# Kernel optimization log

Hardware: AMD Instinct MI355X
Metric: run time of the kernel (lower is better)

## Reference

```python
import jax, jax.numpy as jnp
import numpy as np

B, L, D, ORDER, POS, HID, LMAX = 4, 4096, 1024, 2, 65, 64, 4096
K2 = (POS - 1) // 2

def _layernorm(x, w, b, eps=1e-5):
    m = jnp.mean(x, -1, keepdims=True)
    v = jnp.mean((x - m) ** 2, -1, keepdims=True)
    return (x - m) * jax.lax.rsqrt(v + eps) * w + b

def _fftconv(x, h, d):
    # torch: rfft(h, 2L, norm='forward') * rfft(x, 2L) -> irfft(.., norm='forward')
    # net scaling equals standard (unnormalized fwd / 1-over-n inverse) circular conv,
    # which is exactly jnp.fft default conventions.
    n = 2 * x.shape[-1]
    y = jnp.fft.irfft(jnp.fft.rfft(x, n=n) * jnp.fft.rfft(h, n=n), n=n)[..., : x.shape[-1]]
    return y + x * d

def setup_inputs() -> dict:
    key = jax.random.key(0)
    ks = jax.random.split(key, 12)
    s = 0.05
    # PositionalEncoding buffers/params (deterministic init, as in torch __init__)
    t = np.linspace(0, 1, LMAX, dtype=np.float64)[:, None]
    t_pos = np.arange(LMAX, dtype=np.float64)[:, None]
    k = np.arange(K2, dtype=np.float64)[None, :]
    z = np.exp(1j * 2 * np.pi * k * t_pos / LMAX)
    pos_z = np.concatenate([t, z.real, z.imag], axis=-1).astype(np.float32)  # (LMAX, POS)
    pos_t = t.reshape(1, 1, LMAX).astype(np.float32)
    # ExponentialDecayWindow alphas (deterministic init)
    max_decay = np.log(0.01) / 0.3
    min_decay = np.log(0.01) / 1.5
    alphas = np.linspace(min_decay, max_decay, D).reshape(1, D, 1).astype(np.float32)
    H3 = (ORDER + 1) * D
    return dict(
        u=jax.random.normal(ks[0], (B, L, D), jnp.float32),
        norm1_w=jnp.ones((D,), jnp.float32), norm1_b=jnp.zeros((D,), jnp.float32),
        proj_w=jax.random.normal(ks[1], (H3, D), jnp.float32) * s,
        proj_b=jnp.zeros((H3,), jnp.float32),
        conv_w=jax.random.normal(ks[2], (H3, 1, 3), jnp.float32) * 0.3,
        conv_b=jnp.zeros((H3,), jnp.float32),
        pos_t=jnp.asarray(pos_t), pos_z=jnp.asarray(pos_z),
        fnn_w0=jax.random.normal(ks[3], (HID, POS), jnp.float32) * s,
        fnn_b0=jnp.zeros((HID,), jnp.float32),
        freq0=8.0 * jnp.ones((1, HID), jnp.float32),
        fnn_w1=jax.random.normal(ks[4], (HID, HID), jnp.float32) * s,
        fnn_b1=jnp.zeros((HID,), jnp.float32),
        freq1=8.0 * jnp.ones((1, HID), jnp.float32),
        fnn_w2=jax.random.normal(ks[5], (HID, HID), jnp.float32) * s,
        fnn_b2=jnp.zeros((HID,), jnp.float32),
        freq2=8.0 * jnp.ones((1, HID), jnp.float32),
        fnn_wout=jax.random.normal(ks[6], (ORDER * D, HID), jnp.float32) * s,
        alphas=jnp.asarray(alphas),
        hy_bias=jax.random.normal(ks[7], (ORDER, 1, D, 1), jnp.float32),
        norm2_w=jnp.ones((D,), jnp.float32), norm2_b=jnp.zeros((D,), jnp.float32),
        fc_w=jax.random.normal(ks[8], (D, D), jnp.float32) * s,
        fc_b=jnp.zeros((D,), jnp.float32),
    )

def reference(u, norm1_w, norm1_b, proj_w, proj_b, conv_w, conv_b, pos_t, pos_z,
              fnn_w0, fnn_b0, freq0, fnn_w1, fnn_b1, freq1, fnn_w2, fnn_b2, freq2,
              fnn_wout, alphas, hy_bias, norm2_w, norm2_b, fc_w, fc_b):
    Lq = u.shape[1]
    # Projection: LN -> Linear -> depthwise short conv (causal-ish, pad=2, slice :L)
    x = _layernorm(u, norm1_w, norm1_b)
    x = jnp.einsum('bld,hd->blh', x, proj_w) + proj_b          # (B,L,3D)
    x = x.transpose(0, 2, 1)                                   # (B,3D,L)
    x = jax.lax.conv_general_dilated(
        x, conv_w, window_strides=(1,), padding=[(2, 2)],
        feature_group_count=x.shape[1],
        dimension_numbers=('NCH', 'OIH', 'NCH'))[..., :Lq] + conv_b[None, :, None]
    # HyenaFilter: sin-MLP over positional features, then exp-decay window
    zf = pos_z[:Lq]                                            # (L,POS)
    h = jnp.sin(freq0 * (zf @ fnn_w0.T + fnn_b0))
    h = jnp.sin(freq1 * (h @ fnn_w1.T + fnn_b1))
    h = jnp.sin(freq2 * (h @ fnn_w2.T + fnn_b2))
    h = (h @ fnn_wout.T).T.reshape(ORDER, D, Lq)               # (order,D,L)
    decay = jnp.exp(alphas * pos_t[..., :Lq])                  # (1,D,L)
    h = h * decay
    # order-wise gated FFT long convolution (faithful to torch chunk/broadcast semantics)
    v = x[:, -1:, :]                                           # (B,1,L)
    for i in range(ORDER):
        v = x[:, i:i + 1, :] * _fftconv(v, h[i][None], hy_bias[i])  # (B,D,L)
    y = u + v.transpose(0, 2, 1)
    out = _layernorm(y, norm2_w, norm2_b) @ fc_w.T + fc_b      # activation = identity
    return out + y
```

## Files before the change

### kernel.cpp

```cpp
#include <hip/hip_runtime.h>
#include <hip/hip_bf16.h>

#define LL 4096
#define DD 1024
#define NB 4
#define N4 4096
#define KBINS 4097
#define NSLOT4 4366
#define PI_F 3.14159265358979323846f
#define INV4 (1.0f / 4096.0f)

typedef __attribute__((ext_vector_type(4))) float f32x4;
typedef __attribute__((ext_vector_type(8))) short s16x8;

__device__ __forceinline__ unsigned short f2bf(float f) {
  unsigned int x = __float_as_uint(f);
  x += 0x7fffu + ((x >> 16) & 1u);
  return (unsigned short)(x >> 16);
}

__device__ __forceinline__ int SLT(int n) { return n + (n >> 4) + (n >> 8); }
__device__ __forceinline__ int brev12(int n) { return (int)(__brev((unsigned)n) >> 20); }

__device__ __forceinline__ float2 cmul(float2 a, float2 b) {
  return make_float2(a.x * b.x - a.y * b.y, a.x * b.y + a.y * b.x);
}
__device__ __forceinline__ float2 cadd(float2 a, float2 b) { return make_float2(a.x + b.x, a.y + b.y); }
__device__ __forceinline__ float2 csub(float2 a, float2 b) { return make_float2(a.x - b.x, a.y - b.y); }
__device__ __forceinline__ float2 conjf(float2 a) { return make_float2(a.x, -a.y); }
__device__ __forceinline__ float2 mulni(float2 v) { return make_float2(v.y, -v.x); }
__device__ __forceinline__ float2 mulpi(float2 v) { return make_float2(-v.y, v.x); }

__global__ void k_twiddle(float2* tw) {
  int k = blockIdx.x * 256 + threadIdx.x;
  if (k < 4096) {
    float ang = -2.0f * PI_F * (float)k / 8192.0f;
    float s, c;
    sincosf(ang, &s, &c);
    tw[k] = make_float2(c, s);
  }
}

template<bool INV>
__device__ __forceinline__ void bfly8(float2& A0, float2& A1, float2& A2, float2& A3,
                                      float2& A4, float2& A5, float2& A6, float2& A7,
                                      float2 w1, float2 w2, float2 w3) {
  const float C8 = 0.70710678118654752f;
  float2 t;
  t = cmul(w1, A1); float2 b0 = cadd(A0, t), b1 = csub(A0, t);
  t = cmul(w1, A3); float2 b2 = cadd(A2, t), b3 = csub(A2, t);
  t = cmul(w1, A5); float2 b4 = cadd(A4, t), b5 = csub(A4, t);
  t = cmul(w1, A7); float2 b6 = cadd(A6, t), b7 = csub(A6, t);
  t = cmul(w2, b2);                     float2 c0 = cadd(b0, t), c2 = csub(b0, t);
  t = cmul(w2, b3); t = INV ? mulpi(t) : mulni(t);
  float2 c1 = cadd(b1, t), c3 = csub(b1, t);
  t = cmul(w2, b6);                     float2 c4 = cadd(b4, t), c6 = csub(b4, t);
  t = cmul(w2, b7); t = INV ? mulpi(t) : mulni(t);
  float2 c5 = cadd(b5, t), c7 = csub(b5, t);
  t = cmul(w3, c4); A0 = cadd(c0, t); A4 = csub(c0, t);
  float2 e1 = cmul(w3, c5);
  t = INV ? make_float2(C8 * (e1.x - e1.y), C8 * (e1.y + e1.x))
          : make_float2(C8 * (e1.x + e1.y), C8 * (e1.y - e1.x));
  A1 = cadd(c1, t); A5 = csub(c1, t);
  float2 e2 = cmul(w3, c6); t = INV ? mulpi(e2) : mulni(e2);
  A2 = cadd(c2, t); A6 = csub(c2, t);
  float2 e3 = cmul(w3, c7);
  t = INV ? make_float2(-C8 * (e3.x + e3.y), C8 * (e3.x - e3.y))
          : make_float2(C8 * (e3.y - e3.x), -C8 * (e3.x + e3.y));
  A3 = cadd(c3, t); A7 = csub(c3, t);
}

template<bool INV>
__device__ __forceinline__ void fft4k_01(float2* Z, const float2* __restrict__ tw) {
  const int tid = threadIdx.x;
#pragma unroll
  for (int p = 0; p < 3; ++p) {
    const int hs = 3 * p;
    const int h = 1 << hs;
    const int j0 = tid & (h - 1);
    const int i = ((tid >> hs) << (hs + 3)) + j0;
    int s0 = SLT(i),         s1 = SLT(i + h),     s2 = SLT(i + 2 * h), s3 = SLT(i + 3 * h);
    int s4 = SLT(i + 4 * h), s5 = SLT(i + 5 * h), s6 = SLT(i + 6 * h), s7 = SLT(i + 7 * h);
    float2 a0 = Z[s0], a1 = Z[s1], a2 = Z[s2], a3 = Z[s3];
    float2 a4 = Z[s4], a5 = Z[s5], a6 = Z[s6], a7 = Z[s7];
    float2 w1 = tw[j0 << (12 - hs)];
    float2 w2 = tw[j0 << (11 - hs)];
    float2 w3 = tw[j0 << (10 - hs)];
    if (INV) { w1.y = -w1.y; w2.y = -w2.y; w3.y = -w3.y; }
    bfly8<INV>(a0, a1, a2, a3, a4, a5, a6, a7, w1, w2, w3);
    Z[s0] = a0; Z[s1] = a1; Z[s2] = a2; Z[s3] = a3;
    Z[s4] = a4; Z[s5] = a5; Z[s6] = a6; Z[s7] = a7;
    __builtin_amdgcn_wave_barrier();
  }
}

template<bool INV>
__device__ __forceinline__ void fft4k_p3(const float2* Z, const float2* __restrict__ tw,
                                         float2 d[8]) {
  const int t = threadIdx.x;
#pragma unroll
  for (int k = 0; k < 8; ++k) d[k] = Z[SLT(t + 512 * k)];
  float2 w1 = tw[t << 3], w2 = tw[t << 2], w3 = tw[t << 1];
  if (INV) { w1.y = -w1.y; w2.y = -w2.y; w3.y = -w3.y; }
  bfly8<INV>(d[0], d[1], d[2], d[3], d[4], d[5], d[6], d[7], w1, w2, w3);
}

__global__ __launch_bounds__(256) void k_ln_proj(
    const float* __restrict__ u, const float* __restrict__ n1w, const float* __restrict__ n1b,
    const float* __restrict__ pw, const float* __restrict__ pb,
    float* __restrict__ xp0, float* __restrict__ xp1, float* __restrict__ xpL) {
  const int wid = threadIdx.x >> 6, lane = threadIdx.x & 63;
  const int r = blockIdx.x * 4 + wid;
  const float* ur = u + (size_t)r * DD;
  float4 uv[4];
  float s = 0.f, sq = 0.f;
#pragma unroll
  for (int c = 0; c < 4; ++c) {
    uv[c] = ((const float4*)ur)[lane + 64 * c];
    s += uv[c].x + uv[c].y + uv[c].z + uv[c].w;
    sq += uv[c].x * uv[c].x + uv[c].y * uv[c].y + uv[c].z * uv[c].z + uv[c].w * uv[c].w;
  }
  for (int m = 1; m < 64; m <<= 1) { s += __shfl_xor(s, m); sq += __shfl_xor(sq, m); }
  const float mean = s * (1.0f / DD);
  const float var = sq * (1.0f / DD) - mean * mean;
  const float rs = rsqrtf(var + 1e-5f);
  float d0 = 0.f, d1 = 0.f, dL = 0.f;
  const float* pwL = pw + (size_t)3071 * DD;
#pragma unroll
  for (int c = 0; c < 4; ++c) {
    int i4 = lane + 64 * c;
    float4 wv = ((const float4*)n1w)[i4];
    float4 bv = ((const float4*)n1b)[i4];
    float4 p0 = ((const float4*)pw)[i4];
    float4 p1v = ((const float4*)(pw + DD))[i4];
    float4 pLv = ((const float4*)pwL)[i4];
    float xn;
    xn = (uv[c].x - mean) * rs * wv.x + bv.x; d0 += xn * p0.x; d1 += xn * p1v.x; dL += xn * pLv.x;
    xn = (uv[c].y - mean) * rs * wv.y + bv.y; d0 += xn * p0.y; d1 += xn * p1v.y; dL += xn * pLv.y;
    xn = (uv[c].z - mean) * rs * wv.z + bv.z; d0 += xn * p0.z; d1 += xn * p1v.z; dL += xn * pLv.z;
    xn = (uv[c].w - mean) * rs * wv.w + bv.w; d0 += xn * p0.w; d1 += xn * p1v.w; dL += xn * pLv.w;
  }
  for (int m = 1; m < 64; m <<= 1) {
    d0 += __shfl_xor(d0, m); d1 += __shfl_xor(d1, m); dL += __shfl_xor(dL, m);
  }
  if (lane == 0) {
    xp0[r] = d0 + pb[0];
    xp1[r] = d1 + pb[1];
    xpL[r] = dL + pb[3071];
  }
}

__global__ __launch_bounds__(256) void k_tapconv(
    const float* __restrict__ xp0, const float* __restrict__ xp1, const float* __restrict__ xpL,
    const float* __restrict__ cw, const float* __restrict__ cb,
    float* __restrict__ x0c, float* __restrict__ x1c, float* __restrict__ xLc) {
  int idx = blockIdx.x * 256 + threadIdx.x;
  if (idx >= NB * LL) return;
  int l = idx & (LL - 1);
  int base = idx - l;
  {
    const float* a = xp0 + base;
    float v = cw[2] * a[l];
    if (l >= 1) v += cw[1] * a[l - 1];
    if (l >= 2) v += cw[0] * a[l - 2];
    x0c[idx] = v + cb[0];
  }
  {
    const float* a = xp1 + base;
    float v = cw[5] * a[l];
    if (l >= 1) v += cw[4] * a[l - 1];
    if (l >= 2) v += cw[3] * a[l - 2];
    x1c[idx] = v + cb[1];
  }
  {
    const float* a = xpL + base;
    float v = cw[3071 * 3 + 2] * a[l];
    if (l >= 1) v += cw[3071 * 3 + 1] * a[l - 1];
    if (l >= 2) v += cw[3071 * 3 + 0] * a[l - 2];
    xLc[idx] = v + cb[3071];
  }
}

__global__ __launch_bounds__(256) void k_ffn_hidden(
    const float* __restrict__ pos_z,
    const float* __restrict__ w0, const float* __restrict__ b0, const float* __restrict__ f0,
    const float* __restrict__ w1, const float* __restrict__ b1, const float* __restrict__ f1,
    const float* __restrict__ w2, const float* __restrict__ b2, const float* __restrict__ f2,
    float* __restrict__ hid2T) {
  __shared__ float zin[4][66];
  __shared__ float hbuf[4][64];
  const int g = threadIdx.x >> 6, lane = threadIdx.x & 63;
  const int l0 = blockIdx.x * 16;
  for (int it = 0; it < 4; ++it) {
    const int l = l0 + g * 4 + it;
    zin[g][lane] = pos_z[(size_t)l * 65 + lane];
    if (lane == 0) zin[g][64] = pos_z[(size_t)l * 65 + 64];
    __syncthreads();
    float acc = b0[lane];
#pragma unroll
    for (int k = 0; k < 65; ++k) acc += zin[g][k] * w0[lane * 65 + k];
    float hv = sinf(f0[lane] * acc);
    __syncthreads();
    hbuf[g][lane] = hv;
    __syncthreads();
    acc = b1[lane];
#pragma unroll
    for (int k = 0; k < 64; ++k) acc += hbuf[g][k] * w1[lane * 64 + k];
    hv = sinf(f1[lane] * acc);
    __syncthreads();
    hbuf[g][lane] = hv;
    __syncthreads();
    acc = b2[lane];
#pragma unroll
    for (int k = 0; k < 64; ++k) acc += hbuf[g][k] * w2[lane * 64 + k];
    hv = sinf(f2[lane] * acc);
    hid2T[(size_t)lane * LL + l] = hv;
    __syncthreads();
  }
}

__global__ __launch_bounds__(512, 4) void k_fft_filters(
    const float* __restrict__ hid2T, const float* __restrict__ wout,
    const float* __restrict__ alphas, const float* __restrict__ pos_t,
    float2* __restrict__ Hs, const float2* __restrict__ tw) {
  __shared__ float2 Z[NSLOT4];
  __shared__ float wd[64];
  const int i = blockIdx.x >> 10, d = blockIdx.x & 1023;
  const int tid = threadIdx.x;
  if (tid < 64) wd[tid] = wout[(size_t)(i * DD + d) * 64 + tid];
  __syncthreads();
  const float ad = alphas[d];
  const float2* h2 = (const float2*)hid2T;
  const float2* pt2 = (const float2*)pos_t;
#pragma unroll
  for (int gi = 0; gi < 4; ++gi) {
    int j = tid + gi * 512;
    float2 acc = make_float2(0.f, 0.f);
#pragma unroll 16
    for (int k = 0; k < 64; ++k) {
      float2 hv = h2[(size_t)k * 2048 + j];
      acc.x = fmaf(hv.x, wd[k], acc.x);
      acc.y = fmaf(hv.y, wd[k], acc.y);
    }
    float2 tt = pt2[j];
    float2 val = make_float2(acc.x * expf(ad * tt.x), acc.y * expf(ad * tt.y));
    int r = brev12(j);
    Z[SLT(r)] = val;
    Z[SLT(r + 1)] = make_float2(0.f, 0.f);
  }
  __syncthreads();
  fft4k_01<false>(Z, tw);
  __syncthreads();
  float2 dd[8];
  fft4k_p3<false>(Z, tw, dd);
#pragma unroll
  for (int k = 0; k < 8; ++k) Z[SLT(tid + 512 * k)] = dd[k];
  __syncthreads();
  float2* O1 = Hs + ((size_t)i * DD + d) * KBINS;
#pragma unroll
  for (int gi = 0; gi < 4; ++gi) {
    int k = tid + gi * 512;
    float2 zk = Z[SLT(k)];
    float2 zm = Z[SLT((N4 - k) & (N4 - 1))];
    float2 B = conjf(zm);
    float2 E = make_float2(0.5f * (zk.x + B.x), 0.5f * (zk.y + B.y));
    float2 F = make_float2(0.5f * (zk.x - B.x), 0.5f * (zk.y - B.y));
    float2 G = cmul(tw[k], F);
    float2 WO = mulni(G);
    O1[k] = cadd(E, WO);
    O1[N4 - k] = conjf(csub(E, WO));
  }
  if (tid == 0) {
    float2 zc = Z[SLT(2048)];
    float2 F = make_float2(0.f, zc.y);
    float2 G = cmul(tw[2048], F);
    O1[2048] = cadd(make_float2(zc.x, 0.f), mulni(G));
  }
}

__global__ __launch_bounds__(512, 4) void k_fft_v0(const float* __restrict__ xLc,
                                                   float2* __restrict__ V0s,
                                                   const float2* __restrict__ tw) {
  __shared__ float2 Z[NSLOT4];
  const int b = blockIdx.x;
  const int tid = threadIdx.x;
  const float2* src = (const float2*)(xLc + (size_t)b * LL);
#pragma unroll
  for (int gi = 0; gi < 4; ++gi) {
    int j = tid + gi * 512;
    float2 v = src[j];
    int r = brev12(j);
    Z[SLT(r)] = v;
    Z[SLT(r + 1)] = make_float2(0.f, 0.f);
  }
  __syncthreads();
  fft4k_01<false>(Z, tw);
  __syncthreads();
  float2 dd[8];
  fft4k_p3<false>(Z, tw, dd);
#pragma unroll
  for (int k = 0; k < 8; ++k) Z[SLT(tid + 512 * k)] = dd[k];
  __syncthreads();
  float2* Va = V0s + (size_t)b * KBINS;
#pragma unroll
  for (int gi = 0; gi < 4; ++gi) {
    int k = tid + gi * 512;
    float2 zk = Z[SLT(k)];
    float2 zm = Z[SLT((N4 - k) & (N4 - 1))];
    float2 B = conjf(zm);
    float2 E = make_float2(0.5f * (zk.x + B.x), 0.5f * (zk.y + B.y));
    float2 F = make_float2(0.5f * (zk.x - B.x), 0.5f * (zk.y - B.y));
    float2 G = cmul(tw[k], F);
    float2 WO = mulni(G);
    Va[k] = cadd(E, WO);
    Va[N4 - k] = conjf(csub(E, WO));
  }
  if (tid == 0) {
    float2 zc = Z[SLT(2048)];
    float2 F = make_float2(0.f, zc.y);
    float2 G = cmul(tw[2048], F);
    Va[2048] = cadd(make_float2(zc.x, 0.f), mulni(G));
  }
}

__global__ __launch_bounds__(512, 4) void k_conv12(
    const float2* __restrict__ Hs, const float2* __restrict__ V0s,
    const float* __restrict__ x0c, const float* __restrict__ x1c, const float* __restrict__ xLc,
    const float* __restrict__ hyb, float* __restrict__ v2, const float2* __restrict__ tw) {
  __shared__ float2 Z[NSLOT4];
  const int b = blockIdx.x >> 10, d = blockIdx.x & 1023;
  const int tid = threadIdx.x;
  const float2* H0 = Hs + (size_t)d * KBINS;
  const float2* H1 = Hs + (size_t)(DD + d) * KBINS;
  const float2* V = V0s + (size_t)b * KBINS;
#pragma unroll
  for (int gi = 0; gi < 4; ++gi) {
    int k = tid + gi * 512;
    int m = N4 - k;
    float2 Yk = cmul(V[k], H0[k]);
    float2 Ym = cmul(V[m], H0[m]);
    float2 B = conjf(Ym);
    float2 E = make_float2(0.5f * (Yk.x + B.x), 0.5f * (Yk.y + B.y));
    float2 F = make_float2(0.5f * (Yk.x - B.x), 0.5f * (Yk.y - B.y));
    float2 O = cmul(conjf(tw[k]), F);
    float2 iO = mulpi(O);
    Z[SLT(brev12(k))] = cadd(E, iO);
    if (k > 0) Z[SLT(brev12(m))] = conjf(csub(E, iO));
  }
  if (tid == 0) {
    float2 A = cmul(V[2048], H0[2048]);
    float2 F = make_float2(0.f, A.y);
    float2 O = cmul(conjf(tw[2048]), F);
    Z[SLT(brev12(2048))] = cadd(make_float2(A.x, 0.f), mulpi(O));
  }
  __syncthreads();
  fft4k_01<true>(Z, tw);
  __syncthreads();
  float2 dA[8];
  fft4k_p3<true>(Z, tw, dA);
  const float bd0 = hyb[d], bd1 = hyb[DD + d];
  const float2* g0 = (const float2*)(x0c + (size_t)b * LL);
  const float2* g1 = (const float2*)(x1c + (size_t)b * LL);
  const float2* v0 = (const float2*)(xLc + (size_t)b * LL);
  float2 vsave[4];
#pragma unroll
  for (int k = 0; k < 4; ++k) {
    int j = tid + 512 * k;
    float2 gg = g0[j], vv = v0[j];
    vsave[k] = make_float2(gg.x * fmaf(dA[k].x, INV4, bd0 * vv.x),
                           gg.y * fmaf(dA[k].y, INV4, bd0 * vv.y));
  }
  __syncthreads();
#pragma unroll
  for (int k = 0; k < 4; ++k) {
    int j = tid + 512 * k;
    int r = brev12(j);
    Z[SLT(r)] = vsave[k];
    Z[SLT(r + 1)] = make_float2(0.f, 0.f);
  }
  __syncthreads();
  fft4k_01<false>(Z, tw);
  __syncthreads();
  float2 dB[8];
  fft4k_p3<false>(Z, tw, dB);
#pragma unroll
  for (int k = 0; k < 8; ++k) Z[SLT(tid + 512 * k)] = dB[k];
  __syncthreads();
  float2 zpk[4], zpm[4], z2048;
#pragma unroll
  for (int gi = 0; gi < 4; ++gi) {
    int k = tid + gi * 512;
    int m = N4 - k;
    float2 zk = Z[SLT(k)];
    float2 zm = Z[SLT(m & (N4 - 1))];
    float2 B = conjf(zm);
    float2 E = make_float2(0.5f * (zk.x + B.x), 0.5f * (zk.y + B.y));
    float2 F = make_float2(0.5f * (zk.x - B.x), 0.5f * (zk.y - B.y));
    float2 wk = tw[k];
    float2 G = cmul(wk, F);
    float2 WO = mulni(G);
    float2 Xk = cadd(E, WO);
    float2 Xm = conjf(csub(E, WO));
    float2 Yk = cmul(Xk, H1[k]);
    float2 Ym = cmul(Xm, H1[m]);
    float2 B2 = conjf(Ym);
    float2 E2 = make_float2(0.5f * (Yk.x + B2.x), 0.5f * (Yk.y + B2.y));
    float2 F2 = make_float2(0.5f * (Yk.x - B2.x), 0.5f * (Yk.y - B2.y));
    float2 O2 = cmul(conjf(wk), F2);
    float2 iO2 = mulpi(O2);
    zpk[gi] = cadd(E2, iO2);
    zpm[gi] = conjf(csub(E2, iO2));
  }
  if (tid == 0) {
    float2 zc = Z[SLT(2048)];
    float2 F = make_float2(0.f, zc.y);
    float2 G = cmul(tw[2048], F);
    float2 Xk = cadd(make_float2(zc.x, 0.f), mulni(G));
    float2 Y = cmul(Xk, H1[2048]);
    float2 F2 = make_float2(0.f, Y.y);
    float2 O2 = cmul(conjf(tw[2048]), F2);
    z2048 = cadd(make_float2(Y.x, 0.f), mulpi(O2));
  }
  __syncthreads();
#pragma unroll
  for (int gi = 0; gi < 4; ++gi) {
    int k = tid + gi * 512;
    Z[SLT(brev12(k))] = zpk[gi];
    if (k > 0) Z[SLT(brev12(N4 - k))] = zpm[gi];
  }
  if (tid == 0) Z[SLT(brev12(2048))] = z2048;
  __syncthreads();
  fft4k_01<true>(Z, tw);
  __syncthreads();
  float2 dC[8];
  fft4k_p3<true>(Z, tw, dC);
  float2* out2 = (float2*)(v2 + ((size_t)b * DD + d) * LL);
#pragma unroll
  for (int k = 0; k < 4; ++k) {
    int j = tid + 512 * k;
    float2 gg = g1[j];
    out2[j] = make_float2(gg.x * fmaf(dC[k].x, INV4, bd1 * vsave[k].x),
                          gg.y * fmaf(dC[k].y, INV4, bd1 * vsave[k].y));
  }
}

__global__ __launch_bounds__(256) void k_transpose_add(const float* __restrict__ v2,
                                                       const float* __restrict__ u,
                                                       float* __restrict__ y) {
  __shared__ float T[64][65];
  const int bid = blockIdx.x;
  const int lt = bid & 63, dt = (bid >> 6) & 15, b = bid >> 10;
  const int t = threadIdx.x;
  const int tdr = t >> 2, lc0 = (t & 3) * 16;
  const float* vp = v2 + ((size_t)(b * DD + dt * 64 + tdr)) * LL + lt * 64 + lc0;
#pragma unroll
  for (int q = 0; q < 4; ++q) {
    float4 vv = ((const float4*)vp)[q];
    T[tdr][lc0 + 4 * q + 0] = vv.x;
    T[tdr][lc0 + 4 * q + 1] = vv.y;
    T[tdr][lc0 + 4 * q + 2] = vv.z;
    T[tdr][lc0 + 4 * q + 3] = vv.w;
  }
  __syncthreads();
  const int dc = t & 63, lg = t >> 6;
#pragma unroll
  for (int lr0 = 0; lr0 < 64; lr0 += 4) {
    int lr = lr0 + lg;
    size_t idx = ((size_t)b * LL + lt * 64 + lr) * DD + dt * 64 + dc;
    y[idx] = u[idx] + T[dc][lr];
  }
}

__global__ __launch_bounds__(256) void k_ln2(const float* __restrict__ y,
                                             const float* __restrict__ w,
                                             const float* __restrict__ bb,
                                             unsigned short* __restrict__ yln) {
  const int wid = threadIdx.x >> 6, lane = threadIdx.x & 63;
  const size_t r = (size_t)blockIdx.x * 4 + wid;
  const float* yr = y + r * DD;
  float4 v[4];
  float s = 0.f, sq = 0.f;
#pragma unroll
  for (int c = 0; c < 4; ++c) {
    v[c] = ((const float4*)yr)[lane + 64 * c];
    s += v[c].x + v[c].y + v[c].z + v[c].w;
    sq += v[c].x * v[c].x + v[c].y * v[c].y + v[c].z * v[c].z + v[c].w * v[c].w;
  }
  for (int m = 1; m < 64; m <<= 1) { s += __shfl_xor(s, m); sq += __shfl_xor(sq, m); }
  const float mean = s * (1.0f / DD);
  const float var = sq * (1.0f / DD) - mean * mean;
  const float rs = rsqrtf(var + 1e-5f);
#pragma unroll
  for (int c = 0; c < 4; ++c) {
    int i4 = lane + 64 * c;
    float4 wv = ((const float4*)w)[i4];
    float4 bv = ((const float4*)bb)[i4];
    ushort4 o;
    o.x = f2bf((v[c].x - mean) * rs * wv.x + bv.x);
    o.y = f2bf((v[c].y - mean) * rs * wv.y + bv.y);
    o.z = f2bf((v[c].z - mean) * rs * wv.z + bv.z);
    o.w = f2bf((v[c].w - mean) * rs * wv.w + bv.w);
    ((ushort4*)(yln + r * DD))[i4] = o;
  }
}

__global__ void k_cast(const float* __restrict__ src, unsigned short* __restrict__ dst, int n4) {
  int i = blockIdx.x * 256 + threadIdx.x;
  if (i < n4) {
    float4 v = ((const float4*)src)[i];
    ushort4 o;
    o.x = f2bf(v.x); o.y = f2bf(v.y); o.z = f2bf(v.z); o.w = f2bf(v.w);
    ((ushort4*)dst)[i] = o;
  }
}

#define GBM 128
#define GBN 128
#define GBK 64
#define LDKP 72

__global__ __launch_bounds__(256) void k_gemm(const short* __restrict__ A,
                                              const short* __restrict__ Bw,
                                              const float* __restrict__ fcb,
                                              const float* __restrict__ yy,
                                              float* __restrict__ out) {
  __shared__ short As[GBM * LDKP];
  __shared__ short Bs[GBN * LDKP];
  const int t = threadIdx.x;
  const int bm = blockIdx.x & 127;
  const int bn = blockIdx.x >> 7;
  const int wave = t >> 6, lane = t & 63;
  const int wr = wave >> 1, wc = wave & 1;
  const int rrow = lane & 15, kb = (lane >> 4) * 8;

  f32x4 acc[4][4];
#pragma unroll
  for (int i = 0; i < 4; ++i)
#pragma unroll
    for (int j = 0; j < 4; ++j) acc[i][j] = (f32x4){0.f, 0.f, 0.f, 0.f};

  for (int k0 = 0; k0 < 1024; k0 += GBK) {
#pragma unroll
    for (int c = 0; c < 4; ++c) {
      int chunk = c * 256 + t;
      int row = chunk >> 3, off = (chunk & 7) * 8;
      s16x8 av = *(const s16x8*)(A + ((size_t)(bm * GBM + row)) * 1024 + k0 + off);
      *(s16x8*)&As[row * LDKP + off] = av;
      s16x8 bv = *(const s16x8*)(Bw + ((size_t)(bn * GBN + row)) * 1024 + k0 + off);
      *(s16x8*)&Bs[row * LDKP + off] = bv;
    }
    __syncthreads();
    s16x8 af[2][4], bfr[2][4];
#pragma unroll
    for (int ks = 0; ks < 2; ++ks) {
#pragma unroll
      for (int mr = 0; mr < 4; ++mr)
        af[ks][mr] = *(const s16x8*)&As[(wr * 64 + mr * 16 + rrow) * LDKP + ks * 32 + kb];
#pragma unroll
      for (int nc = 0; nc < 4; ++nc)
        bfr[ks][nc] = *(const s16x8*)&Bs[(wc * 64 + nc * 16 + rrow) * LDKP + ks * 32 + kb];
    }
#pragma unroll
    for (int ks = 0; ks < 2; ++ks)
#pragma unroll
      for (int mr = 0; mr < 4; ++mr)
#pragma unroll
        for (int nc = 0; nc < 4; ++nc)
          acc[mr][nc] = __builtin_amdgcn_mfma_f32_16x16x32_bf16(af[ks][mr], bfr[ks][nc],
                                                                acc[mr][nc], 0, 0, 0);
    __syncthreads();
  }
  const int cg = lane >> 4, cr = lane & 15;
#pragma unroll
  for (int mr = 0; mr < 4; ++mr)
#pragma unroll
    for (int nc = 0; nc < 4; ++nc) {
      f32x4 a = acc[mr][nc];
      int col = bn * GBN + wc * 64 + nc * 16 + cr;
#pragma unroll
      for (int q = 0; q < 4; ++q) {
        int row = bm * GBM + wr * 64 + mr * 16 + cg * 4 + q;
        size_t idx = (size_t)row * 1024 + col;
        out[idx] = a[q] + fcb[col] + yy[idx];
      }
    }
}

extern "C" void kernel_launch(void* const* d_in, const int* in_sizes, int n_in,
                              void* d_out, int out_size, void* d_ws, size_t ws_size,
                              hipStream_t stream) {
  const float* u      = (const float*)d_in[0];
  const float* n1w    = (const float*)d_in[1];
  const float* n1b    = (const float*)d_in[2];
  const float* projw  = (const float*)d_in[3];
  const float* projb  = (const float*)d_in[4];
  const float* convw  = (const float*)d_in[5];
  const float* convb  = (const float*)d_in[6];
  const float* pos_t  = (const float*)d_in[7];
  const float* pos_z  = (const float*)d_in[8];
  const float* w0     = (const float*)d_in[9];
  const float* b0     = (const float*)d_in[10];
  const float* f0     = (const float*)d_in[11];
  const float* w1     = (const float*)d_in[12];
  const float* b1     = (const float*)d_in[13];
  const float* f1     = (const float*)d_in[14];
  const float* w2     = (const float*)d_in[15];
  const float* b2     = (const float*)d_in[16];
  const float* f2     = (const float*)d_in[17];
  const float* wout   = (const float*)d_in[18];
  const float* alphas = (const float*)d_in[19];
  const float* hyb    = (const float*)d_in[20];
  const float* n2w    = (const float*)d_in[21];
  const float* n2b    = (const float*)d_in[22];
  const float* fcw    = (const float*)d_in[23];
  const float* fcb    = (const float*)d_in[24];

  char* wsb = (char*)d_ws;
  size_t off = 0;
  auto alloc = [&](size_t bytes) -> void* {
    off = (off + 255) & ~(size_t)255;
    void* p = wsb + off;
    off += bytes;
    return p;
  };
  float2* tw    = (float2*)alloc(sizeof(float2) * 4096);
  float*  xp0   = (float*)alloc(sizeof(float) * NB * LL);
  float*  xp1   = (float*)alloc(sizeof(float) * NB * LL);
  float*  xpL   = (float*)alloc(sizeof(float) * NB * LL);
  float*  x0c   = (float*)alloc(sizeof(float) * NB * LL);
  float*  x1c   = (float*)alloc(sizeof(float) * NB * LL);
  float*  xLc   = (float*)alloc(sizeof(float) * NB * LL);
  float*  hid2T = (float*)alloc(sizeof(float) * 64 * LL);
  float2* Hs    = (float2*)alloc(sizeof(float2) * 2 * DD * KBINS);
  float2* V0s   = (float2*)alloc(sizeof(float2) * NB * KBINS);
  float*  v2    = (float*)alloc(sizeof(float) * NB * DD * LL);
  unsigned short* fcwb = (unsigned short*)alloc(sizeof(unsigned short) * DD * DD);
  float*          y   = (float*)Hs;
  unsigned short* yln = (unsigned short*)v2;
  (void)ws_size; (void)in_sizes; (void)n_in; (void)out_size;

  k_twiddle<<<16, 256, 0, stream>>>(tw);
  k_ln_proj<<<(NB * LL) / 4, 256, 0, stream>>>(u, n1w, n1b, projw, projb, xp0, xp1, xpL);
  k_tapconv<<<(NB * LL) / 256, 256, 0, stream>>>(xp0, xp1, xpL, convw, convb, x0c, x1c, xLc);
  k_ffn_hidden<<<LL / 16, 256, 0, stream>>>(pos_z, w0, b0, f0, w1, b1, f1, w2, b2, f2, hid2T);
  k_fft_filters<<<2048, 512, 0, stream>>>(hid2T, wout, alphas, pos_t, Hs, tw);
  k_fft_v0<<<NB, 512, 0, stream>>>(xLc, V0s, tw);
  k_conv12<<<NB * DD, 512, 0, stream>>>(Hs, V0s, x0c, x1c, xLc, hyb, v2, tw);
  k_transpose_add<<<4096, 256, 0, stream>>>(v2, u, y);
  k_ln2<<<(NB * LL) / 4, 256, 0, stream>>>(y, n2w, n2b, yln);
  k_cast<<<(DD * DD / 4) / 256, 256, 0, stream>>>(fcw, fcwb, DD * DD / 4);
  k_gemm<<<(16384 / GBM) * (1024 / GBN), 256, 0, stream>>>((const short*)yln, (const short*)fcwb,
                                                           fcb, y, (float*)d_out);
}
```

Measured before the change: 445.4 us.

## Restructure 4K FFTs as radix-16 passes with 256 threads and XOR swizzle

Replaces the radix-8, three-pass shared-memory FFT (512 threads, padded layout) with radix-16 butterflies over 256 threads, using an XOR-swizzled 4096-entry LDS layout. The first radix-16 stage runs in registers with unit twiddles and the zero padding folded in, and some values stay in registers instead of round-tripping through LDS. This aims to cut LDS traffic, passes and barriers in the filter, v0 and conv kernels. In exchange each thread holds more registers (16-element arrays), which may lower occupancy, and the index mapping is intricate and easy to get subtly wrong.

```diff
diff --git a/kernel.cpp b/kernel.cpp
--- a/kernel.cpp
+++ b/kernel.cpp
@@ -6,7 +6,6 @@
 #define NB 4
 #define N4 4096
 #define KBINS 4097
-#define NSLOT4 4366
 #define PI_F 3.14159265358979323846f
 #define INV4 (1.0f / 4096.0f)
 
@@ -19,8 +18,9 @@
   return (unsigned short)(x >> 16);
 }
 
-__device__ __forceinline__ int SLT(int n) { return n + (n >> 4) + (n >> 8); }
+__device__ __forceinline__ int SX(int n) { return n ^ ((n >> 4) & 15); }
 __device__ __forceinline__ int brev12(int n) { return (int)(__brev((unsigned)n) >> 20); }
+__device__ __forceinline__ int brev8(int n) { return (int)(__brev((unsigned)n) >> 24); }
 
 __device__ __forceinline__ float2 cmul(float2 a, float2 b) {
   return make_float2(a.x * b.x - a.y * b.y, a.x * b.y + a.y * b.x);
@@ -71,38 +71,73 @@
 }
 
 template<bool INV>
-__device__ __forceinline__ void fft4k_01(float2* Z, const float2* __restrict__ tw) {
-  const int tid = threadIdx.x;
-#pragma unroll
-  for (int p = 0; p < 3; ++p) {
-    const int hs = 3 * p;
-    const int h = 1 << hs;
-    const int j0 = tid & (h - 1);
-    const int i = ((tid >> hs) << (hs + 3)) + j0;
-    int s0 = SLT(i),         s1 = SLT(i + h),     s2 = SLT(i + 2 * h), s3 = SLT(i + 3 * h);
-    int s4 = SLT(i + 4 * h), s5 = SLT(i + 5 * h), s6 = SLT(i + 6 * h), s7 = SLT(i + 7 * h);
-    float2 a0 = Z[s0], a1 = Z[s1], a2 = Z[s2], a3 = Z[s3];
-    float2 a4 = Z[s4], a5 = Z[s5], a6 = Z[s6], a7 = Z[s7];
-    float2 w1 = tw[j0 << (12 - hs)];
-    float2 w2 = tw[j0 << (11 - hs)];
-    float2 w3 = tw[j0 << (10 - hs)];
-    if (INV) { w1.y = -w1.y; w2.y = -w2.y; w3.y = -w3.y; }
-    bfly8<INV>(a0, a1, a2, a3, a4, a5, a6, a7, w1, w2, w3);
-    Z[s0] = a0; Z[s1] = a1; Z[s2] = a2; Z[s3] = a3;
-    Z[s4] = a4; Z[s5] = a5; Z[s6] = a6; Z[s7] = a7;
-    __builtin_amdgcn_wave_barrier();
-  }
+__device__ __forceinline__ void bfly16(float2 x[16], float2 w1, float2 w2, float2 w3, float2 w4) {
+  bfly8<INV>(x[0], x[1], x[2], x[3], x[4], x[5], x[6], x[7], w1, w2, w3);
+  bfly8<INV>(x[8], x[9], x[10], x[11], x[12], x[13], x[14], x[15], w1, w2, w3);
+  const float C8 = 0.70710678118654752f;
+  const float c16 = 0.92387953251128676f, s16 = 0.38268343236508977f;
+  float2 t;
+  t = cmul(w4, x[8]);
+  x[8] = csub(x[0], t); x[0] = cadd(x[0], t);
+  t = cmul(w4, x[9]);
+  t = INV ? make_float2(c16 * t.x - s16 * t.y, c16 * t.y + s16 * t.x)
+          : make_float2(c16 * t.x + s16 * t.y, c16 * t.y - s16 * t.x);
+  x[9] = csub(x[1], t); x[1] = cadd(x[1], t);
+  t = cmul(w4, x[10]);
+  t = INV ? make_float2(C8 * (t.x - t.y), C8 * (t.y + t.x))
+          : make_float2(C8 * (t.x + t.y), C8 * (t.y - t.x));
+  x[10] = csub(x[2], t); x[2] = cadd(x[2], t);
+  t = cmul(w4, x[11]);
+  t = INV ? make_float2(s16 * t.x - c16 * t.y, s16 * t.y + c16 * t.x)
+          : make_float2(s16 * t.x + c16 * t.y, s16 * t.y - c16 * t.x);
+  x[11] = csub(x[3], t); x[3] = cadd(x[3], t);
+  t = cmul(w4, x[12]);
+  t = INV ? mulpi(t) : mulni(t);
+  x[12] = csub(x[4], t); x[4] = cadd(x[4], t);
+  t = cmul(w4, x[13]);
+  t = INV ? make_float2(-s16 * t.x - c16 * t.y, -s16 * t.y + c16 * t.x)
+          : make_float2(-s16 * t.x + c16 * t.y, -s16 * t.y - c16 * t.x);
+  x[13] = csub(x[5], t); x[5] = cadd(x[5], t);
+  t = cmul(w4, x[14]);
+  t = INV ? make_float2(-C8 * (t.x + t.y), C8 * (t.x - t.y))
+          : make_float2(C8 * (t.y - t.x), -C8 * (t.x + t.y));
+  x[14] = csub(x[6], t); x[6] = cadd(x[6], t);
+  t = cmul(w4, x[15]);
+  t = INV ? make_float2(-c16 * t.x - s16 * t.y, -c16 * t.y + s16 * t.x)
+          : make_float2(-c16 * t.x + s16 * t.y, -c16 * t.y - s16 * t.x);
+  x[15] = csub(x[7], t); x[7] = cadd(x[7], t);
 }
 
 template<bool INV>
-__device__ __forceinline__ void fft4k_p3(const float2* Z, const float2* __restrict__ tw,
-                                         float2 d[8]) {
+__device__ __forceinline__ void pass1_16(float2* Z, const float2* __restrict__ tw) {
   const int t = threadIdx.x;
-#pragma unroll
-  for (int k = 0; k < 8; ++k) d[k] = Z[SLT(t + 512 * k)];
-  float2 w1 = tw[t << 3], w2 = tw[t << 2], w3 = tw[t << 1];
-  if (INV) { w1.y = -w1.y; w2.y = -w2.y; w3.y = -w3.y; }
-  bfly8<INV>(d[0], d[1], d[2], d[3], d[4], d[5], d[6], d[7], w1, w2, w3);
+  const int j0 = t & 15;
+  const int i = ((t >> 4) << 8) + j0;
+  float2 x[16];
+#pragma unroll
+  for (int q = 0; q < 16; ++q) x[q] = Z[SX(i + 16 * q)];
+  float2 w1 = tw[j0 << 8], w2 = tw[j0 << 7], w3 = tw[j0 << 6], w4 = tw[j0 << 5];
+  if (INV) { w1.y = -w1.y; w2.y = -w2.y; w3.y = -w3.y; w4.y = -w4.y; }
+  bfly16<INV>(x, w1, w2, w3, w4);
+#pragma unroll
+  for (int q = 0; q < 16; ++q) Z[SX(i + 16 * q)] = x[q];
+}
+
+template<bool INV>
+__device__ __forceinline__ void pass2_16(const float2* Z, const float2* __restrict__ tw,
+                                         float2 x[16]) {
+  const int t = threadIdx.x;
+#pragma unroll
+  for (int q = 0; q < 16; ++q) x[q] = Z[SX(t + 256 * q)];
+  float2 w1 = tw[t << 4], w2 = tw[t << 3], w3 = tw[t << 2], w4 = tw[t << 1];
+  if (INV) { w1.y = -w1.y; w2.y = -w2.y; w3.y = -w3.y; w4.y = -w4.y; }
+  bfly16<INV>(x, w1, w2, w3, w4);
+}
+
+#define UNIT make_float2(1.f, 0.f)
+__device__ __forceinline__ constexpr int rev4q(int q) {
+  return (q == 0) ? 0 : (q == 1) ? 8 : (q == 2) ? 4 : (q == 3) ? 12
+       : (q == 4) ? 2 : (q == 5) ? 10 : (q == 6) ? 6 : 14;
 }
 
 __global__ __launch_bounds__(256) void k_ln_proj(
@@ -219,22 +254,24 @@
   }
 }
 
-__global__ __launch_bounds__(512, 4) void k_fft_filters(
+__global__ __launch_bounds__(256) void k_fft_filters(
     const float* __restrict__ hid2T, const float* __restrict__ wout,
     const float* __restrict__ alphas, const float* __restrict__ pos_t,
     float2* __restrict__ Hs, const float2* __restrict__ tw) {
-  __shared__ float2 Z[NSLOT4];
+  __shared__ float2 Z[4096];
   __shared__ float wd[64];
   const int i = blockIdx.x >> 10, d = blockIdx.x & 1023;
-  const int tid = threadIdx.x;
-  if (tid < 64) wd[tid] = wout[(size_t)(i * DD + d) * 64 + tid];
+  const int t = threadIdx.x;
+  const int rr = brev8(t);
+  if (t < 64) wd[t] = wout[(size_t)(i * DD + d) * 64 + t];
   __syncthreads();
   const float ad = alphas[d];
   const float2* h2 = (const float2*)hid2T;
   const float2* pt2 = (const float2*)pos_t;
-#pragma unroll
-  for (int gi = 0; gi < 4; ++gi) {
-    int j = tid + gi * 512;
+  float2 pv[8];
+#pragma unroll
+  for (int g = 0; g < 8; ++g) {
+    int j = t + 256 * g;
     float2 acc = make_float2(0.f, 0.f);
 #pragma unroll 16
     for (int k = 0; k < 64; ++k) {
@@ -243,25 +280,36 @@
       acc.y = fmaf(hv.y, wd[k], acc.y);
     }
     float2 tt = pt2[j];
-    float2 val = make_float2(acc.x * expf(ad * tt.x), acc.y * expf(ad * tt.y));
-    int r = brev12(j);
-    Z[SLT(r)] = val;
-    Z[SLT(r + 1)] = make_float2(0.f, 0.f);
-  }
-  __syncthreads();
-  fft4k_01<false>(Z, tw);
-  __syncthreads();
-  float2 dd[8];
-  fft4k_p3<false>(Z, tw, dd);
-#pragma unroll
-  for (int k = 0; k < 8; ++k) Z[SLT(tid + 512 * k)] = dd[k];
+    pv[g] = make_float2(acc.x * expf(ad * tt.x), acc.y * expf(ad * tt.y));
+  }
+#pragma unroll
+  for (int g = 0; g < 8; ++g) Z[SX(16 * rr + rev4q(g))] = pv[g];
+  __syncthreads();
+  {
+    float2 x[16];
+#pragma unroll
+    for (int jj = 0; jj < 8; ++jj) {
+      x[2 * jj] = Z[SX(16 * t + 2 * jj)];
+      x[2 * jj + 1] = make_float2(0.f, 0.f);
+    }
+    bfly16<false>(x, UNIT, UNIT, UNIT, UNIT);
+#pragma unroll
+    for (int j = 0; j < 16; ++j) Z[SX(16 * t + j)] = x[j];
+  }
+  __builtin_amdgcn_wave_barrier();
+  pass1_16<false>(Z, tw);
+  __syncthreads();
+  float2 dd[16];
+  pass2_16<false>(Z, tw, dd);
+#pragma unroll
+  for (int q = 0; q < 16; ++q) Z[SX(t + 256 * q)] = dd[q];
   __syncthreads();
   float2* O1 = Hs + ((size_t)i * DD + d) * KBINS;
 #pragma unroll
-  for (int gi = 0; gi < 4; ++gi) {
-    int k = tid + gi * 512;
-    float2 zk = Z[SLT(k)];
-    float2 zm = Z[SLT((N4 - k) & (N4 - 1))];
+  for (int q = 0; q < 8; ++q) {
+    int k = t + 256 * q;
+    float2 zk = dd[q];
+    float2 zm = Z[SX((N4 - k) & (N4 - 1))];
     float2 B = conjf(zm);
     float2 E = make_float2(0.5f * (zk.x + B.x), 0.5f * (zk.y + B.y));
     float2 F = make_float2(0.5f * (zk.x - B.x), 0.5f * (zk.y - B.y));
@@ -270,43 +318,50 @@
     O1[k] = cadd(E, WO);
     O1[N4 - k] = conjf(csub(E, WO));
   }
-  if (tid == 0) {
-    float2 zc = Z[SLT(2048)];
+  if (t == 0) {
+    float2 zc = dd[8];
     float2 F = make_float2(0.f, zc.y);
     float2 G = cmul(tw[2048], F);
     O1[2048] = cadd(make_float2(zc.x, 0.f), mulni(G));
   }
 }
 
-__global__ __launch_bounds__(512, 4) void k_fft_v0(const float* __restrict__ xLc,
-                                                   float2* __restrict__ V0s,
-                                                   const float2* __restrict__ tw) {
-  __shared__ float2 Z[NSLOT4];
+__global__ __launch_bounds__(256) void k_fft_v0(const float* __restrict__ xLc,
+                                                float2* __restrict__ V0s,
+                                                const float2* __restrict__ tw) {
+  __shared__ float2 Z[4096];
   const int b = blockIdx.x;
-  const int tid = threadIdx.x;
+  const int t = threadIdx.x;
+  const int rr = brev8(t);
   const float2* src = (const float2*)(xLc + (size_t)b * LL);
 #pragma unroll
-  for (int gi = 0; gi < 4; ++gi) {
-    int j = tid + gi * 512;
-    float2 v = src[j];
-    int r = brev12(j);
-    Z[SLT(r)] = v;
-    Z[SLT(r + 1)] = make_float2(0.f, 0.f);
-  }
-  __syncthreads();
-  fft4k_01<false>(Z, tw);
-  __syncthreads();
-  float2 dd[8];
-  fft4k_p3<false>(Z, tw, dd);
-#pragma unroll
-  for (int k = 0; k < 8; ++k) Z[SLT(tid + 512 * k)] = dd[k];
+  for (int g = 0; g < 8; ++g) Z[SX(16 * rr + rev4q(g))] = src[t + 256 * g];
+  __syncthreads();
+  {
+    float2 x[16];
+#pragma unroll
+    for (int jj = 0; jj < 8; ++jj) {
+      x[2 * jj] = Z[SX(16 * t + 2 * jj)];
+      x[2 * jj + 1] = make_float2(0.f, 0.f);
+    }
+    bfly16<false>(x, UNIT, UNIT, UNIT, UNIT);
+#pragma unroll
+    for (int j = 0; j < 16; ++j) Z[SX(16 * t + j)] = x[j];
+  }
+  __builtin_amdgcn_wave_barrier();
+  pass1_16<false>(Z, tw);
+  __syncthreads();
+  float2 dd[16];
+  pass2_16<false>(Z, tw, dd);
+#pragma unroll
+  for (int q = 0; q < 16; ++q) Z[SX(t + 256 * q)] = dd[q];
   __syncthreads();
   float2* Va = V0s + (size_t)b * KBINS;
 #pragma unroll
-  for (int gi = 0; gi < 4; ++gi) {
-    int k = tid + gi * 512;
-    float2 zk = Z[SLT(k)];
-    float2 zm = Z[SLT((N4 - k) & (N4 - 1))];
+  for (int q = 0; q < 8; ++q) {
+    int k = t + 256 * q;
+    float2 zk = dd[q];
+    float2 zm = Z[SX((N4 - k) & (N4 - 1))];
     float2 B = conjf(zm);
     float2 E = make_float2(0.5f * (zk.x + B.x), 0.5f * (zk.y + B.y));
     float2 F = make_float2(0.5f * (zk.x - B.x), 0.5f * (zk.y - B.y));
@@ -315,27 +370,30 @@
     Va[k] = cadd(E, WO);
     Va[N4 - k] = conjf(csub(E, WO));
   }
-  if (tid == 0) {
-    float2 zc = Z[SLT(2048)];
+  if (t == 0) {
+    float2 zc = dd[8];
     float2 F = make_float2(0.f, zc.y);
     float2 G = cmul(tw[2048], F);
     Va[2048] = cadd(make_float2(zc.x, 0.f), mulni(G));
   }
 }
 
-__global__ __launch_bounds__(512, 4) void k_conv12(
+__global__ __launch_bounds__(256) void k_conv12(
     const float2* __restrict__ Hs, const float2* __restrict__ V0s,
     const float* __restrict__ x0c, const float* __restrict__ x1c, const float* __restrict__ xLc,
     const float* __restrict__ hyb, float* __restrict__ v2, const float2* __restrict__ tw) {
-  __shared__ float2 Z[NSLOT4];
+  __shared__ float2 Z[4096];
   const int b = blockIdx.x >> 10, d = blockIdx.x & 1023;
-  const int tid = threadIdx.x;
+  const int t = threadIdx.x;
+  const int rr = brev8(t);
   const float2* H0 = Hs + (size_t)d * KBINS;
   const float2* H1 = Hs + (size_t)(DD + d) * KBINS;
   const float2* V = V0s + (size_t)b * KBINS;
-#pragma unroll
-  for (int gi = 0; gi < 4; ++gi) {
-    int k = tid + gi * 512;
+  float2 xA[16];
+  float2 w2048A = make_float2(0.f, 0.f);
+#pragma unroll
+  for (int q = 0; q < 8; ++q) {
+    int k = rr + 256 * q;
     int m = N4 - k;
     float2 Yk = cmul(V[k], H0[k]);
     float2 Ym = cmul(V[m], H0[m]);
@@ -344,55 +402,69 @@
     float2 F = make_float2(0.5f * (Yk.x - B.x), 0.5f * (Yk.y - B.y));
     float2 O = cmul(conjf(tw[k]), F);
     float2 iO = mulpi(O);
-    Z[SLT(brev12(k))] = cadd(E, iO);
-    if (k > 0) Z[SLT(brev12(m))] = conjf(csub(E, iO));
-  }
-  if (tid == 0) {
+    xA[rev4q(q)] = cadd(E, iO);
+    if (k > 0) Z[SX(brev12(m))] = conjf(csub(E, iO));
+  }
+  if (t == 0) {
     float2 A = cmul(V[2048], H0[2048]);
     float2 F = make_float2(0.f, A.y);
     float2 O = cmul(conjf(tw[2048]), F);
-    Z[SLT(brev12(2048))] = cadd(make_float2(A.x, 0.f), mulpi(O));
-  }
-  __syncthreads();
-  fft4k_01<true>(Z, tw);
-  __syncthreads();
-  float2 dA[8];
-  fft4k_p3<true>(Z, tw, dA);
+    w2048A = cadd(make_float2(A.x, 0.f), mulpi(O));
+  }
+  __syncthreads();
+#pragma unroll
+  for (int jj = 0; jj < 8; ++jj) xA[2 * jj + 1] = Z[SX(16 * t + 2 * jj + 1)];
+  if (t == 0) xA[1] = w2048A;
+  bfly16<true>(xA, UNIT, UNIT, UNIT, UNIT);
+#pragma unroll
+  for (int j = 0; j < 16; ++j) Z[SX(16 * t + j)] = xA[j];
+  __builtin_amdgcn_wave_barrier();
+  pass1_16<true>(Z, tw);
+  __syncthreads();
+  float2 dA[16];
+  pass2_16<true>(Z, tw, dA);
   const float bd0 = hyb[d], bd1 = hyb[DD + d];
   const float2* g0 = (const float2*)(x0c + (size_t)b * LL);
   const float2* g1 = (const float2*)(x1c + (size_t)b * LL);
   const float2* v0 = (const float2*)(xLc + (size_t)b * LL);
-  float2 vsave[4];
-#pragma unroll
-  for (int k = 0; k < 4; ++k) {
-    int j = tid + 512 * k;
+  float2 vsave[8];
+#pragma unroll
+  for (int q = 0; q < 8; ++q) {
+    int j = t + 256 * q;
     float2 gg = g0[j], vv = v0[j];
-    vsave[k] = make_float2(gg.x * fmaf(dA[k].x, INV4, bd0 * vv.x),
-                           gg.y * fmaf(dA[k].y, INV4, bd0 * vv.y));
-  }
-  __syncthreads();
-#pragma unroll
-  for (int k = 0; k < 4; ++k) {
-    int j = tid + 512 * k;
-    int r = brev12(j);
-    Z[SLT(r)] = vsave[k];
-    Z[SLT(r + 1)] = make_float2(0.f, 0.f);
-  }
-  __syncthreads();
-  fft4k_01<false>(Z, tw);
-  __syncthreads();
-  float2 dB[8];
-  fft4k_p3<false>(Z, tw, dB);
-#pragma unroll
-  for (int k = 0; k < 8; ++k) Z[SLT(tid + 512 * k)] = dB[k];
-  __syncthreads();
-  float2 zpk[4], zpm[4], z2048;
-#pragma unroll
-  for (int gi = 0; gi < 4; ++gi) {
-    int k = tid + gi * 512;
+    vsave[q] = make_float2(gg.x * fmaf(dA[q].x, INV4, bd0 * vv.x),
+                           gg.y * fmaf(dA[q].y, INV4, bd0 * vv.y));
+  }
+  __syncthreads();
+#pragma unroll
+  for (int q = 0; q < 8; ++q) Z[SX(16 * rr + rev4q(q))] = vsave[q];
+  __syncthreads();
+  {
+    float2 x[16];
+#pragma unroll
+    for (int jj = 0; jj < 8; ++jj) {
+      x[2 * jj] = Z[SX(16 * t + 2 * jj)];
+      x[2 * jj + 1] = make_float2(0.f, 0.f);
+    }
+    bfly16<false>(x, UNIT, UNIT, UNIT, UNIT);
+#pragma unroll
+    for (int j = 0; j < 16; ++j) Z[SX(16 * t + j)] = x[j];
+  }
+  __builtin_amdgcn_wave_barrier();
+  pass1_16<false>(Z, tw);
+  __syncthreads();
+  float2 dB[16];
+  pass2_16<false>(Z, tw, dB);
+#pragma unroll
+  for (int q = 0; q < 16; ++q) Z[SX(t + 256 * q)] = dB[q];
+  __syncthreads();
+  float2 zpk[8], zpm[8], z2048 = make_float2(0.f, 0.f);
+#pragma unroll
+  for (int q = 0; q < 8; ++q) {
+    int k = rr + 256 * q;
     int m = N4 - k;
-    float2 zk = Z[SLT(k)];
-    float2 zm = Z[SLT(m & (N4 - 1))];
+    float2 zk = Z[SX(k)];
+    float2 zm = Z[SX(m & (N4 - 1))];
     float2 B = conjf(zm);
     float2 E = make_float2(0.5f * (zk.x + B.x), 0.5f * (zk.y + B.y));
     float2 F = make_float2(0.5f * (zk.x - B.x), 0.5f * (zk.y - B.y));
@@ -408,11 +480,11 @@
     float2 F2 = make_float2(0.5f * (Yk.x - B2.x), 0.5f * (Yk.y - B2.y));
     float2 O2 = cmul(conjf(wk), F2);
     float2 iO2 = mulpi(O2);
-    zpk[gi] = cadd(E2, iO2);
-    zpm[gi] = conjf(csub(E2, iO2));
-  }
-  if (tid == 0) {
-    float2 zc = Z[SLT(2048)];
+    zpk[q] = cadd(E2, iO2);
+    zpm[q] = conjf(csub(E2, iO2));
+  }
+  if (t == 0) {
+    float2 zc = dB[8];
     float2 F = make_float2(0.f, zc.y);
     float2 G = cmul(tw[2048], F);
     float2 Xk = cadd(make_float2(zc.x, 0.f), mulni(G));
@@ -423,24 +495,34 @@
   }
   __syncthreads();
 #pragma unroll
-  for (int gi = 0; gi < 4; ++gi) {
-    int k = tid + gi * 512;
-    Z[SLT(brev12(k))] = zpk[gi];
-    if (k > 0) Z[SLT(brev12(N4 - k))] = zpm[gi];
-  }
-  if (tid == 0) Z[SLT(brev12(2048))] = z2048;
-  __syncthreads();
-  fft4k_01<true>(Z, tw);
-  __syncthreads();
-  float2 dC[8];
-  fft4k_p3<true>(Z, tw, dC);
+  for (int q = 0; q < 8; ++q) {
+    int k = rr + 256 * q;
+    if (k > 0) Z[SX(brev12(N4 - k))] = zpm[q];
+  }
+  __syncthreads();
+  {
+    float2 x[16];
+#pragma unroll
+    for (int q = 0; q < 8; ++q) x[rev4q(q)] = zpk[q];
+#pragma unroll
+    for (int jj = 0; jj < 8; ++jj) x[2 * jj + 1] = Z[SX(16 * t + 2 * jj + 1)];
+    if (t == 0) x[1] = z2048;
+    bfly16<true>(x, UNIT, UNIT, UNIT, UNIT);
+#pragma unroll
+    for (int j = 0; j < 16; ++j) Z[SX(16 * t + j)] = x[j];
+  }
+  __builtin_amdgcn_wave_barrier();
+  pass1_16<true>(Z, tw);
+  __syncthreads();
+  float2 dC[16];
+  pass2_16<true>(Z, tw, dC);
   float2* out2 = (float2*)(v2 + ((size_t)b * DD + d) * LL);
 #pragma unroll
-  for (int k = 0; k < 4; ++k) {
-    int j = tid + 512 * k;
+  for (int q = 0; q < 8; ++q) {
+    int j = t + 256 * q;
     float2 gg = g1[j];
-    out2[j] = make_float2(gg.x * fmaf(dC[k].x, INV4, bd1 * vsave[k].x),
-                          gg.y * fmaf(dC[k].y, INV4, bd1 * vsave[k].y));
+    out2[j] = make_float2(gg.x * fmaf(dC[q].x, INV4, bd1 * vsave[q].x),
+                          gg.y * fmaf(dC[q].y, INV4, bd1 * vsave[q].y));
   }
 }
 
@@ -643,9 +725,9 @@
   k_ln_proj<<<(NB * LL) / 4, 256, 0, stream>>>(u, n1w, n1b, projw, projb, xp0, xp1, xpL);
   k_tapconv<<<(NB * LL) / 256, 256, 0, stream>>>(xp0, xp1, xpL, convw, convb, x0c, x1c, xLc);
   k_ffn_hidden<<<LL / 16, 256, 0, stream>>>(pos_z, w0, b0, f0, w1, b1, f1, w2, b2, f2, hid2T);
-  k_fft_filters<<<2048, 512, 0, stream>>>(hid2T, wout, alphas, pos_t, Hs, tw);
-  k_fft_v0<<<NB, 512, 0, stream>>>(xLc, V0s, tw);
-  k_conv12<<<NB * DD, 512, 0, stream>>>(Hs, V0s, x0c, x1c, xLc, hyb, v2, tw);
+  k_fft_filters<<<2048, 256, 0, stream>>>(hid2T, wout, alphas, pos_t, Hs, tw);
+  k_fft_v0<<<NB, 256, 0, stream>>>(xLc, V0s, tw);
+  k_conv12<<<NB * DD, 256, 0, stream>>>(Hs, V0s, x0c, x1c, xLc, hyb, v2, tw);
   k_transpose_add<<<4096, 256, 0, stream>>>(v2, u, y);
   k_ln2<<<(NB * LL) / 4, 256, 0, stream>>>(y, n2w, n2b, yln);
   k_cast<<<(DD * DD / 4) / 256, 256, 0, stream>>>(fcw, fcwb, DD * DD / 4);
```

After: 498.1 us. +11.9%, slower.
